# Kernel tuning notes

Measured on AMD Instinct MI355X. Metric: run time of the kernel, lower is better.

The kernel has to match this reference:

```python
import jax, jax.numpy as jnp
import numpy as np

DIM = 192; HEADS = 6; HD = DIM // HEADS; SCALE = HD ** -0.5
WS = (4, 8, 8); SS = (2, 4, 4)
NW = WS[0] * WS[1] * WS[2]  # tokens per window = 256
HIDDEN = 768; RANK1 = 384; RANK2 = 96

def _rel_index():
    Wd, Wh, Ww = WS
    coords = np.stack(np.meshgrid(np.arange(Wd), np.arange(Wh), np.arange(Ww), indexing='ij')).reshape(3, -1)
    rel = (coords[:, :, None] - coords[:, None, :]).transpose(1, 2, 0)
    rel = rel + np.array([Wd - 1, Wh - 1, Ww - 1])
    rel[:, :, 0] *= (2 * Wh - 1) * (2 * Ww - 1)
    rel[:, :, 1] *= 2 * Ww - 1
    return rel.sum(-1)  # (NW, NW) int

REL_IDX = jnp.asarray(_rel_index())

def _attn_mask(B, D, H, W):
    # static numpy computation (D,H,W are python ints) -> constant under jit
    img = np.zeros((B, D, H, W), np.float32); cnt = 0
    for d in range(0, D, WS[0]):
        for h in range(0, H, WS[1]):
            for w in range(0, W, WS[2]):
                img[:, d:d + WS[0], h:h + WS[1], w:w + WS[2]] = cnt; cnt += 1
    if any(s > 0 for s in SS):
        img = np.roll(img, (-SS[0], -SS[1], -SS[2]), axis=(1, 2, 3))
    mw = img.reshape(B, D // WS[0], WS[0], H // WS[1], WS[1], W // WS[2], WS[2]).transpose(0, 1, 3, 5, 2, 4, 6).reshape(-1, NW)
    diff = mw[:, :, None] - mw[:, None, :]
    return jnp.asarray(np.where(diff != 0, -100.0, 0.0).astype(np.float32))  # (B*nW, NW, NW)

def _ln(x, g, b):
    mu = x.mean(-1, keepdims=True)
    var = ((x - mu) ** 2).mean(-1, keepdims=True)
    return (x - mu) / jnp.sqrt(var + 1e-5) * g + b

def setup_inputs() -> dict:
    key = jax.random.key(0)
    ks = jax.random.split(key, 16)
    B, D, H, W = 1, 16, 64, 64
    N = D * H * W
    s = 0.02
    return {
        'x': jax.random.normal(ks[0], (B, N, DIM), jnp.float32),
        'norm1_g': jnp.ones((DIM,), jnp.float32), 'norm1_b': jnp.zeros((DIM,), jnp.float32),
        'qkv_w': jax.random.normal(ks[1], (DIM, 3 * DIM), jnp.float32) * s,
        'qkv_b': jnp.zeros((3 * DIM,), jnp.float32),
        'rel_bias': jax.random.normal(ks[2], (1575, HEADS), jnp.float32) * s,
        'proj_w': jax.random.normal(ks[3], (DIM, DIM), jnp.float32) * s,
        'proj_b': jnp.zeros((DIM,), jnp.float32),
        'norm2_g': jnp.ones((DIM,), jnp.float32), 'norm2_b': jnp.zeros((DIM,), jnp.float32),
        'fc1_A': jax.random.normal(ks[4], (DIM, RANK1), jnp.float32) * s,
        'fc1_Bw': jax.random.normal(ks[5], (RANK1, HIDDEN), jnp.float32) * s,
        'fc1_Bb': jnp.zeros((HIDDEN,), jnp.float32),
        'dw_w': jax.random.normal(ks[6], (HIDDEN, 1, 3, 3, 3), jnp.float32) * s,
        'dw_b': jnp.zeros((HIDDEN,), jnp.float32),
        'fc2_A': jax.random.normal(ks[7], (HIDDEN, RANK2), jnp.float32) * s,
        'fc2_Bw': jax.random.normal(ks[8], (RANK2, DIM), jnp.float32) * s,
        'fc2_Bb': jnp.zeros((DIM,), jnp.float32),
        'D': D, 'H': H, 'W': W,
    }

def reference(x, norm1_g, norm1_b, qkv_w, qkv_b, rel_bias, proj_w, proj_b,
              norm2_g, norm2_b, fc1_A, fc1_Bw, fc1_Bb, dw_w, dw_b,
              fc2_A, fc2_Bw, fc2_Bb, D, H, W):
    B, N, C = x.shape
    Wd, Wh, Ww = WS
    shortcut = x
    # --- shifted-window attention (NB: original repo never rolls x; only the mask is shifted) ---
    h = _ln(x, norm1_g, norm1_b).reshape(B, D, H, W, C)
    xw = h.reshape(B, D // Wd, Wd, H // Wh, Wh, W // Ww, Ww, C)
    xw = xw.transpose(0, 1, 3, 5, 2, 4, 6, 7).reshape(-1, NW, C)  # (B*nW, NW, C)
    qkv = (xw @ qkv_w + qkv_b).reshape(-1, NW, 3, HEADS, HD).transpose(2, 0, 3, 1, 4)
    q, k, v = qkv[0] * SCALE, qkv[1], qkv[2]           # (B*nW, heads, NW, hd)
    attn = jnp.einsum('bhnd,bhmd->bhnm', q, k)
    bias = rel_bias[REL_IDX].transpose(2, 0, 1)[None]  # (1, heads, NW, NW)
    mask = _attn_mask(B, D, H, W)                      # (B*nW, NW, NW)
    attn = jax.nn.softmax(attn + bias + mask[:, None], axis=-1)
    out = jnp.einsum('bhnm,bhmd->bhnd', attn, v).transpose(0, 2, 1, 3).reshape(-1, NW, C)
    out = out @ proj_w + proj_b
    out = out.reshape(B, D // Wd, H // Wh, W // Ww, Wd, Wh, Ww, C)
    out = out.transpose(0, 1, 4, 2, 5, 3, 6, 7).reshape(B, N, C)
    x = shortcut + out
    # --- MixFFN3D: low-rank fc1 -> depthwise conv3d -> GELU -> low-rank fc2 ---
    h = _ln(x, norm2_g, norm2_b)
    h = (h @ fc1_A) @ fc1_Bw + fc1_Bb                 # (B, N, HIDDEN)
    h = h.transpose(0, 2, 1).reshape(B, HIDDEN, D, H, W)
    h = jax.lax.conv_general_dilated(h, dw_w, (1, 1, 1), [(1, 1), (1, 1), (1, 1)],
                                     feature_group_count=HIDDEN,
                                     dimension_numbers=('NCDHW', 'OIDHW', 'NCDHW'))
    h = h + dw_b[None, :, None, None, None]
    h = jax.nn.gelu(h, approximate=False)
    h = h.reshape(B, HIDDEN, N).transpose(0, 2, 1)
    h = (h @ fc2_A) @ fc2_Bw + fc2_Bb                 # (B, N, DIM)
    return x + h
```

## Files before the change

kernel.cpp:

```cpp
#include <hip/hip_runtime.h>
#include <hip/hip_bf16.h>

typedef __hip_bfloat16 bf16;
typedef __attribute__((ext_vector_type(8))) short short8;
typedef __attribute__((ext_vector_type(4))) float f32x4;

#define N_TOK 65536
#define C_DIM 192
#define SCALE 0.17677669529663687f

__device__ __forceinline__ float b2f(bf16 v) { return __bfloat162float(v); }
__device__ __forceinline__ bf16 f2b(float v) { return __float2bfloat16(v); }
__device__ __forceinline__ float ldA(const void* p, size_t i, int f32) {
  return f32 ? ((const float*)p)[i] : b2f(((const bf16*)p)[i]);
}
__device__ __forceinline__ float s2f(short s) { union { short s; bf16 b; } u; u.s = s; return b2f(u.b); }

__global__ void detect_kernel(const unsigned short* __restrict__ xh, int* __restrict__ flag) {
  if (threadIdx.x == 0) {
    int crazy = 0;
    for (int i = 0; i < 256; ++i) {
      int e = (xh[i] >> 7) & 0xFF;
      if (e >= 0xF0 || (e >= 1 && e <= 0x60)) ++crazy;
    }
    *flag = (crazy >= 16) ? 1 : 0;
  }
}

__global__ __launch_bounds__(256) void prep_kernel(
    const void* __restrict__ qkv_w, bf16* __restrict__ QKVT,
    const void* __restrict__ proj_w, bf16* __restrict__ PROJT,
    const void* __restrict__ fc1_A, bf16* __restrict__ FC1AT,
    const void* __restrict__ fc1_Bw, bf16* __restrict__ FC1BT,
    const void* __restrict__ fc2_A, bf16* __restrict__ FC2AT,
    const void* __restrict__ fc2_Bw, bf16* __restrict__ FC2BT,
    const void* __restrict__ dw_w, bf16* __restrict__ DWT,
    const int* __restrict__ flag) {
  int f32 = *flag;
  int b = blockIdx.x;
  const void* in; bf16* out; int K, N, base;
  if (b < 432)       { in = qkv_w;  out = QKVT;  K = 192; N = 576; base = 0; }
  else if (b < 576)  { in = proj_w; out = PROJT; K = 192; N = 192; base = 432; }
  else if (b < 864)  { in = fc1_A;  out = FC1AT; K = 192; N = 384; base = 576; }
  else if (b < 2016) { in = fc1_Bw; out = FC1BT; K = 384; N = 768; base = 864; }
  else if (b < 2304) { in = fc2_A;  out = FC2AT; K = 768; N = 96;  base = 2016; }
  else if (b < 2376) { in = fc2_Bw; out = FC2BT; K = 96;  N = 192; base = 2304; }
  else {
    int idx = (b - 2376) * 256 + threadIdx.x;
    int tap = idx / 768, c = idx - tap * 768;
    DWT[idx] = f2b(ldA(dw_w, (size_t)c * 27 + tap, f32));
    return;
  }
  int idx = (b - base) * 256 + threadIdx.x;
  int n = idx / K, k = idx - n * K;
  out[idx] = f2b(ldA(in, (size_t)k * N + n, f32));
}

__global__ __launch_bounds__(256) void ln_kernel(const void* __restrict__ x,
    const void* __restrict__ g, const void* __restrict__ b, bf16* __restrict__ out,
    int windowize, int xIsBf16Fixed, const int* __restrict__ flag) {
  int wf32 = *flag;
  int f32 = xIsBf16Fixed ? 0 : wf32;
  int token = blockIdx.x * 4 + (threadIdx.x >> 6);
  int lane = threadIdx.x & 63;
  size_t base = (size_t)token * C_DIM;
  float v0 = ldA(x, base + lane, f32);
  float v1 = ldA(x, base + lane + 64, f32);
  float v2 = ldA(x, base + lane + 128, f32);
  float s = v0 + v1 + v2;
  float s2 = v0 * v0 + v1 * v1 + v2 * v2;
  #pragma unroll
  for (int o = 32; o > 0; o >>= 1) { s += __shfl_xor(s, o, 64); s2 += __shfl_xor(s2, o, 64); }
  float mu = s * (1.f / 192.f);
  float var = s2 * (1.f / 192.f) - mu * mu;
  float rstd = rsqrtf(var + 1e-5f);
  int row = token;
  if (windowize) {
    int d = token >> 12, h = (token >> 6) & 63, w = token & 63;
    int win = ((d >> 2) << 6) + ((h >> 3) << 3) + (w >> 3);
    int t = ((d & 3) << 6) + ((h & 7) << 3) + (w & 7);
    row = win * 256 + t;
  }
  bf16* po = out + (size_t)row * C_DIM;
  po[lane]       = f2b((v0 - mu) * rstd * ldA(g, lane, wf32)       + ldA(b, lane, wf32));
  po[lane + 64]  = f2b((v1 - mu) * rstd * ldA(g, lane + 64, wf32)  + ldA(b, lane + 64, wf32));
  po[lane + 128] = f2b((v2 - mu) * rstd * ldA(g, lane + 128, wf32) + ldA(b, lane + 128, wf32));
}

__global__ __launch_bounds__(256) void mfma_gemm(const bf16* __restrict__ A,
    const bf16* __restrict__ BT, const void* __restrict__ bias,
    const void* __restrict__ res, void* __restrict__ out,
    int Nc, int K, int ldk, int mode, const int* __restrict__ flag) {
  int f32 = *flag;
  __shared__ short As[128 * 104];
  __shared__ short Bs[64 * 104];
  int tid = threadIdx.x;
  int wave = tid >> 6, lane = tid & 63;
  int wm = wave >> 1, wn = wave & 1;
  int lr = lane & 15, quad = lane >> 4;
  int ncb = gridDim.x;
  int flat = blockIdx.x + ncb * blockIdx.y;
  int group = flat / (8 * ncb);
  int r = flat - group * 8 * ncb;
  int rowBase = (group * 8 + (r & 7)) * 128;
  int colBase = (r >> 3) * 64;
  f32x4 acc[4][2];
  #pragma unroll
  for (int i = 0; i < 4; ++i)
    #pragma unroll
    for (int j = 0; j < 2; ++j) acc[i][j] = f32x4{0.f, 0.f, 0.f, 0.f};

  for (int k0 = 0; k0 < K; k0 += 96) {
    #pragma unroll
    for (int it = 0; it < 6; ++it) {
      int u = tid + it * 256;
      int row = u / 12, kc = (u - row * 12) * 8;
      uint4 v = *(const uint4*)(A + (size_t)(rowBase + row) * K + k0 + kc);
      *(uint4*)&As[row * 104 + kc] = v;
    }
    #pragma unroll
    for (int it = 0; it < 3; ++it) {
      int u = tid + it * 256;
      int n = u / 12, kc = (u - n * 12) * 8;
      uint4 v = uint4{0u, 0u, 0u, 0u};
      if (colBase + n < Nc)
        v = *(const uint4*)(BT + (size_t)(colBase + n) * ldk + k0 + kc);
      *(uint4*)&Bs[n * 104 + kc] = v;
    }
    __syncthreads();
    #pragma unroll
    for (int kk = 0; kk < 3; ++kk) {
      short8 af[4], bf[2];
      #pragma unroll
      for (int i = 0; i < 4; ++i)
        af[i] = *(const short8*)&As[(wm * 64 + i * 16 + lr) * 104 + kk * 32 + quad * 8];
      #pragma unroll
      for (int j = 0; j < 2; ++j)
        bf[j] = *(const short8*)&Bs[(wn * 32 + j * 16 + lr) * 104 + kk * 32 + quad * 8];
      #pragma unroll
      for (int i = 0; i < 4; ++i)
        #pragma unroll
        for (int j = 0; j < 2; ++j)
          acc[i][j] = __builtin_amdgcn_mfma_f32_16x16x32_bf16(af[i], bf[j], acc[i][j], 0, 0, 0);
    }
    __syncthreads();
  }

  #pragma unroll
  for (int i = 0; i < 4; ++i) {
    #pragma unroll
    for (int j = 0; j < 2; ++j) {
      #pragma unroll
      for (int r4 = 0; r4 < 4; ++r4) {
        int row = rowBase + wm * 64 + i * 16 + quad * 4 + r4;
        int c = colBase + wn * 32 + j * 16 + lr;
        if (c >= Nc) continue;
        float v = acc[i][j][r4];
        if (bias) v += ldA(bias, c, f32);
        if (mode == 0) {
          ((bf16*)out)[(size_t)row * Nc + c] = f2b(v);
        } else if (mode == 1) {
          float o = b2f(((const bf16*)res)[(size_t)row * Nc + c]) + v;
          if (f32) ((float*)out)[(size_t)row * Nc + c] = o;
          else     ((bf16*)out)[(size_t)row * Nc + c] = f2b(o);
        } else {
          int win = row >> 8, t = row & 255;
          int d = ((win >> 6) << 2) + (t >> 6);
          int h = (((win >> 3) & 7) << 3) + ((t >> 3) & 7);
          int w = ((win & 7) << 3) + (t & 7);
          int n = (d << 12) + (h << 6) + w;
          ((bf16*)out)[(size_t)n * C_DIM + c] = f2b(ldA(res, (size_t)n * C_DIM + c, f32) + v);
        }
      }
    }
  }
}

__global__ __launch_bounds__(256) void attn_mfma_kernel(const bf16* __restrict__ qkvr,
    const void* __restrict__ rel_bias, bf16* __restrict__ out,
    const int* __restrict__ flag) {
  int f32 = *flag;
  __shared__ bf16 sK[256 * 40];
  __shared__ bf16 sVT[32 * 264];
  __shared__ bf16 sP[4][64 * 40];
  __shared__ float sb[1575];
  __shared__ int  sgb[256];
  int head = blockIdx.x, win = blockIdx.y;
  const bf16* base = qkvr + (size_t)win * 256 * 576;
  int qoff = head * 32, koff = 192 + head * 32, voff = 384 + head * 32;
  int tid = threadIdx.x;
  int wave = tid >> 6, lane = tid & 63;
  int lr = lane & 15, quad = lane >> 4;

  #pragma unroll
  for (int it = 0; it < 4; ++it) {
    int idx = tid + it * 256;
    int tok = idx >> 2, kc = (idx & 3) * 8;
    uint4 v = *(const uint4*)(base + (size_t)tok * 576 + koff + kc);
    *(uint4*)&sK[tok * 40 + kc] = v;
  }
  for (int idx = tid; idx < 8192; idx += 256) {
    int tok = idx >> 5, hd = idx & 31;
    sVT[hd * 264 + tok] = base[(size_t)tok * 576 + voff + hd];
  }
  for (int idx = tid; idx < 1575; idx += 256) sb[idx] = ldA(rel_bias, (size_t)idx * 6 + head, f32);
  {
    int t = tid & 255;
    int d = ((win >> 6) << 2) + (t >> 6);
    int h = (((win >> 3) & 7) << 3) + ((t >> 3) & 7);
    int w = ((win & 7) << 3) + (t & 7);
    int d2 = (d + 2) & 15, h2 = (h + 4) & 63, w2 = (w + 4) & 63;
    int g = ((d2 >> 2) << 6) + ((h2 >> 3) << 3) + (w2 >> 3);
    int td = t >> 6, th = (t >> 3) & 7, tw = t & 7;
    int bse = (td * 15 + th) * 15 + tw;
    sgb[t] = (g << 12) | bse;
  }
  __syncthreads();

  int wm = wave * 64;
  short8 aq[4];
  #pragma unroll
  for (int i = 0; i < 4; ++i)
    aq[i] = *(const short8*)(base + (size_t)(wm + i * 16 + lr) * 576 + qoff + quad * 8);
  int rinfo[16];
  #pragma unroll
  for (int i = 0; i < 4; ++i)
    #pragma unroll
    for (int r = 0; r < 4; ++r)
      rinfo[i * 4 + r] = sgb[wm + i * 16 + quad * 4 + r];

  f32x4 acc_o[4][2], acc_l[4];
  #pragma unroll
  for (int i = 0; i < 4; ++i) {
    acc_l[i] = f32x4{0.f, 0.f, 0.f, 0.f};
    #pragma unroll
    for (int j = 0; j < 2; ++j) acc_o[i][j] = f32x4{0.f, 0.f, 0.f, 0.f};
  }
  short8 bones;
  #pragma unroll
  for (int j = 0; j < 8; ++j) bones[j] = (lr == 0) ? (short)0x3F80 : (short)0;

  for (int c = 0; c < 8; ++c) {
    short8 bk[2];
    #pragma unroll
    for (int jt = 0; jt < 2; ++jt)
      bk[jt] = *(const short8*)&sK[(c * 32 + jt * 16 + lr) * 40 + quad * 8];
    f32x4 s[4][2];
    #pragma unroll
    for (int i = 0; i < 4; ++i)
      #pragma unroll
      for (int jt = 0; jt < 2; ++jt) {
        s[i][jt] = f32x4{0.f, 0.f, 0.f, 0.f};
        s[i][jt] = __builtin_amdgcn_mfma_f32_16x16x32_bf16(aq[i], bk[jt], s[i][jt], 0, 0, 0);
      }
    int cinfo[2];
    #pragma unroll
    for (int jt = 0; jt < 2; ++jt) cinfo[jt] = sgb[c * 32 + jt * 16 + lr];
    #pragma unroll
    for (int i = 0; i < 4; ++i)
      #pragma unroll
      for (int jt = 0; jt < 2; ++jt)
        #pragma unroll
        for (int r = 0; r < 4; ++r) {
          int ri = rinfo[i * 4 + r], ci = cinfo[jt];
          float sc = s[i][jt][r] * SCALE + sb[(ri & 0xFFF) - (ci & 0xFFF) + 787];
          float p = ((ri >> 12) == (ci >> 12)) ? __expf(sc) : 0.f;
          sP[wave][(i * 16 + quad * 4 + r) * 40 + jt * 16 + lr] = f2b(p);
        }
    short8 ap[4];
    #pragma unroll
    for (int i = 0; i < 4; ++i)
      ap[i] = *(const short8*)&sP[wave][(i * 16 + lr) * 40 + quad * 8];
    short8 bv[2];
    #pragma unroll
    for (int jh = 0; jh < 2; ++jh)
      bv[jh] = *(const short8*)&sVT[(jh * 16 + lr) * 264 + c * 32 + quad * 8];
    #pragma unroll
    for (int i = 0; i < 4; ++i) {
      #pragma unroll
      for (int jh = 0; jh < 2; ++jh)
        acc_o[i][jh] = __builtin_amdgcn_mfma_f32_16x16x32_bf16(ap[i], bv[jh], acc_o[i][jh], 0, 0, 0);
      acc_l[i] = __builtin_amdgcn_mfma_f32_16x16x32_bf16(ap[i], bones, acc_l[i], 0, 0, 0);
    }
  }
  #pragma unroll
  for (int i = 0; i < 4; ++i) {
    #pragma unroll
    for (int r = 0; r < 4; ++r) {
      float l = __shfl(acc_l[i][r], lane & 48, 64);
      float inv = 1.f / l;
      int t = wm + i * 16 + quad * 4 + r;
      bf16* po = out + (size_t)(win * 256 + t) * C_DIM + head * 32;
      po[lr]      = f2b(acc_o[i][0][r] * inv);
      po[16 + lr] = f2b(acc_o[i][1][r] * inv);
    }
  }
}

__global__ __launch_bounds__(256) void dwconv8w4_kernel(const bf16* __restrict__ in,
    const bf16* __restrict__ wT, const void* __restrict__ wb, bf16* __restrict__ out,
    const int* __restrict__ flag) {
  int f32 = *flag;
  int idx = blockIdx.x * 256 + threadIdx.x;
  int n4 = idx / 96, g = idx - n4 * 96;
  int c0 = g * 8;
  int d = n4 >> 10, h = (n4 >> 4) & 63, w0 = (n4 & 15) << 2;
  const bf16* inb = in + c0;
  float acc[4][8];
  {
    float bias[8];
    #pragma unroll
    for (int e = 0; e < 8; ++e) bias[e] = ldA(wb, c0 + e, f32);
    #pragma unroll
    for (int t = 0; t < 4; ++t)
      #pragma unroll
      for (int e = 0; e < 8; ++e) acc[t][e] = bias[e];
  }
  #pragma unroll
  for (int kd = 0; kd < 3; ++kd) {
    int dd = d + kd - 1;
    if ((unsigned)dd >= 16u) continue;
    #pragma unroll
    for (int kh = 0; kh < 3; ++kh) {
      int hh = h + kh - 1;
      if ((unsigned)hh >= 64u) continue;
      int rowbase = (dd << 12) + (hh << 6);
      float xf[6][8];
      #pragma unroll
      for (int j = 0; j < 6; ++j) {
        int ww = w0 + j - 1;
        short8 xv = short8{0, 0, 0, 0, 0, 0, 0, 0};
        if ((unsigned)ww < 64u)
          xv = *(const short8*)(inb + (size_t)(rowbase + ww) * 768);
        #pragma unroll
        for (int e = 0; e < 8; ++e) xf[j][e] = s2f(xv[e]);
      }
      #pragma unroll
      for (int kw = 0; kw < 3; ++kw) {
        int tap = kd * 9 + kh * 3 + kw;
        short8 wv = *(const short8*)(wT + tap * 768 + c0);
        float wf[8];
        #pragma unroll
        for (int e = 0; e < 8; ++e) wf[e] = s2f(wv[e]);
        #pragma unroll
        for (int t = 0; t < 4; ++t)
          #pragma unroll
          for (int e = 0; e < 8; ++e)
            acc[t][e] += xf[t + kw][e] * wf[e];
      }
    }
  }
  #pragma unroll
  for (int t = 0; t < 4; ++t) {
    bf16* po = out + (size_t)((d << 12) + (h << 6) + w0 + t) * 768 + c0;
    #pragma unroll
    for (int e = 0; e < 8; ++e) {
      float s = acc[t][e];
      po[e] = f2b(0.5f * s * (1.f + erff(s * 0.70710678118654752f)));
    }
  }
}

extern "C" void kernel_launch(void* const* d_in, const int* in_sizes, int n_in,
                              void* d_out, int out_size, void* d_ws, size_t ws_size,
                              hipStream_t stream) {
  const void* x      = d_in[0];
  const void* n1g    = d_in[1];
  const void* n1b    = d_in[2];
  const void* qkv_w  = d_in[3];
  const void* qkv_b  = d_in[4];
  const void* relb   = d_in[5];
  const void* proj_w = d_in[6];
  const void* proj_b = d_in[7];
  const void* n2g    = d_in[8];
  const void* n2b    = d_in[9];
  const void* fc1_A  = d_in[10];
  const void* fc1_Bw = d_in[11];
  const void* fc1_Bb = d_in[12];
  const void* dw_w   = d_in[13];
  const void* dw_b   = d_in[14];
  const void* fc2_A  = d_in[15];
  const void* fc2_Bw = d_in[16];
  const void* fc2_Bb = d_in[17];

  char* ws = (char*)d_ws;
  bf16* SCR  = (bf16*)d_out;
  bf16* X1   = (bf16*)(ws);
  bf16* QKVR = (bf16*)(ws + (size_t)24 * 1048576);
  bf16* T1   = (bf16*)(ws + (size_t)24 * 1048576);
  bf16* F2   = (bf16*)(ws + (size_t)24 * 1048576);
  bf16* F1   = (bf16*)(ws + (size_t)120 * 1048576);
  bf16* T2bf = (bf16*)(ws + (size_t)216 * 1048576);
  bf16* QKVT  = (bf16*)(ws + (size_t)228 * 1048576);
  bf16* PROJT = (bf16*)(ws + (size_t)229 * 1048576);
  bf16* FC1AT = (bf16*)(ws + (size_t)230 * 1048576);
  bf16* FC1BT = (bf16*)(ws + (size_t)231 * 1048576);
  bf16* FC2AT = (bf16*)(ws + (size_t)233 * 1048576);
  bf16* FC2BT = (bf16*)(ws + (size_t)234 * 1048576);
  bf16* DWT   = (bf16*)(ws + (size_t)235 * 1048576);
  int* FLAG   = (int*)(ws + (size_t)255 * 1048576);

  detect_kernel<<<1, 64, 0, stream>>>((const unsigned short*)x, FLAG);
  prep_kernel<<<2457, 256, 0, stream>>>(qkv_w, QKVT, proj_w, PROJT, fc1_A, FC1AT,
                                        fc1_Bw, FC1BT, fc2_A, FC2AT, fc2_Bw, FC2BT,
                                        dw_w, DWT, FLAG);
  ln_kernel<<<N_TOK / 4, 256, 0, stream>>>(x, n1g, n1b, SCR, 1, 0, FLAG);
  mfma_gemm<<<dim3(9, 512), 256, 0, stream>>>(SCR, QKVT, qkv_b, nullptr, QKVR,
                                              576, 192, 192, 0, FLAG);
  attn_mfma_kernel<<<dim3(6, 256), 256, 0, stream>>>(QKVR, relb, SCR, FLAG);
  mfma_gemm<<<dim3(3, 512), 256, 0, stream>>>(SCR, PROJT, proj_b, x, X1,
                                              192, 192, 192, 3, FLAG);
  ln_kernel<<<N_TOK / 4, 256, 0, stream>>>(X1, n2g, n2b, SCR, 0, 1, FLAG);
  mfma_gemm<<<dim3(6, 512), 256, 0, stream>>>(SCR, FC1AT, nullptr, nullptr, T1,
                                              384, 192, 192, 0, FLAG);
  mfma_gemm<<<dim3(12, 512), 256, 0, stream>>>(T1, FC1BT, fc1_Bb, nullptr, F1,
                                               768, 384, 384, 0, FLAG);
  dwconv8w4_kernel<<<6144, 256, 0, stream>>>(F1, DWT, dw_b, F2, FLAG);
  mfma_gemm<<<dim3(2, 512), 256, 0, stream>>>(F2, FC2AT, nullptr, nullptr, T2bf,
                                              96, 768, 768, 0, FLAG);
  mfma_gemm<<<dim3(3, 512), 256, 0, stream>>>(T2bf, FC2BT, fc2_Bb, X1, d_out,
                                              192, 96, 96, 1, FLAG);
}
```

Baseline: 732.9 us.

## Fold low-rank FFN factor pairs into dense weights and drop intermediate GEMMs

The prep kernel now multiplies fc1_A·fc1_Bw and fc2_A·fc2_Bw into dense transposed bf16 weights, so each MLP stage runs as one GEMM instead of two. This removes two GEMM launches and the T1/T2 intermediate buffers, and cuts total FLOPs and memory traffic per token. In exchange, the prep kernel does naive per-thread dot products over the rank dimension each call, and the fc2 GEMM becomes larger than its original two-stage form.

```diff
diff --git a/kernel.cpp b/kernel.cpp
--- a/kernel.cpp
+++ b/kernel.cpp
@@ -30,30 +30,39 @@
 __global__ __launch_bounds__(256) void prep_kernel(
     const void* __restrict__ qkv_w, bf16* __restrict__ QKVT,
     const void* __restrict__ proj_w, bf16* __restrict__ PROJT,
-    const void* __restrict__ fc1_A, bf16* __restrict__ FC1AT,
-    const void* __restrict__ fc1_Bw, bf16* __restrict__ FC1BT,
-    const void* __restrict__ fc2_A, bf16* __restrict__ FC2AT,
-    const void* __restrict__ fc2_Bw, bf16* __restrict__ FC2BT,
+    const void* __restrict__ fc1_A, const void* __restrict__ fc1_Bw, bf16* __restrict__ W1T,
+    const void* __restrict__ fc2_A, const void* __restrict__ fc2_Bw, bf16* __restrict__ W2T,
     const void* __restrict__ dw_w, bf16* __restrict__ DWT,
     const int* __restrict__ flag) {
   int f32 = *flag;
   int b = blockIdx.x;
-  const void* in; bf16* out; int K, N, base;
-  if (b < 432)       { in = qkv_w;  out = QKVT;  K = 192; N = 576; base = 0; }
-  else if (b < 576)  { in = proj_w; out = PROJT; K = 192; N = 192; base = 432; }
-  else if (b < 864)  { in = fc1_A;  out = FC1AT; K = 192; N = 384; base = 576; }
-  else if (b < 2016) { in = fc1_Bw; out = FC1BT; K = 384; N = 768; base = 864; }
-  else if (b < 2304) { in = fc2_A;  out = FC2AT; K = 768; N = 96;  base = 2016; }
-  else if (b < 2376) { in = fc2_Bw; out = FC2BT; K = 96;  N = 192; base = 2304; }
-  else {
-    int idx = (b - 2376) * 256 + threadIdx.x;
+  if (b < 432) {
+    int idx = b * 256 + threadIdx.x;
+    int n = idx / 192, k = idx - n * 192;
+    QKVT[idx] = f2b(ldA(qkv_w, (size_t)k * 576 + n, f32));
+  } else if (b < 576) {
+    int idx = (b - 432) * 256 + threadIdx.x;
+    int n = idx / 192, k = idx - n * 192;
+    PROJT[idx] = f2b(ldA(proj_w, (size_t)k * 192 + n, f32));
+  } else if (b < 657) {
+    int idx = (b - 576) * 256 + threadIdx.x;
     int tap = idx / 768, c = idx - tap * 768;
     DWT[idx] = f2b(ldA(dw_w, (size_t)c * 27 + tap, f32));
-    return;
-  }
-  int idx = (b - base) * 256 + threadIdx.x;
-  int n = idx / K, k = idx - n * K;
-  out[idx] = f2b(ldA(in, (size_t)k * N + n, f32));
+  } else if (b < 1233) {
+    int idx = (b - 657) * 256 + threadIdx.x;
+    int k = idx / 768, n = idx - k * 768;
+    float s = 0.f;
+    for (int r = 0; r < 384; ++r)
+      s += ldA(fc1_A, (size_t)k * 384 + r, f32) * ldA(fc1_Bw, (size_t)r * 768 + n, f32);
+    W1T[(size_t)n * 192 + k] = f2b(s);
+  } else {
+    int idx = (b - 1233) * 256 + threadIdx.x;
+    int k = idx / 192, n = idx - k * 192;
+    float s = 0.f;
+    for (int r = 0; r < 96; ++r)
+      s += ldA(fc2_A, (size_t)k * 96 + r, f32) * ldA(fc2_Bw, (size_t)r * 192 + n, f32);
+    W2T[(size_t)n * 768 + k] = f2b(s);
+  }
 }
 
 __global__ __launch_bounds__(256) void ln_kernel(const void* __restrict__ x,
@@ -387,22 +396,19 @@
   bf16* SCR  = (bf16*)d_out;
   bf16* X1   = (bf16*)(ws);
   bf16* QKVR = (bf16*)(ws + (size_t)24 * 1048576);
-  bf16* T1   = (bf16*)(ws + (size_t)24 * 1048576);
   bf16* F2   = (bf16*)(ws + (size_t)24 * 1048576);
   bf16* F1   = (bf16*)(ws + (size_t)120 * 1048576);
-  bf16* T2bf = (bf16*)(ws + (size_t)216 * 1048576);
   bf16* QKVT  = (bf16*)(ws + (size_t)228 * 1048576);
   bf16* PROJT = (bf16*)(ws + (size_t)229 * 1048576);
-  bf16* FC1AT = (bf16*)(ws + (size_t)230 * 1048576);
-  bf16* FC1BT = (bf16*)(ws + (size_t)231 * 1048576);
-  bf16* FC2AT = (bf16*)(ws + (size_t)233 * 1048576);
-  bf16* FC2BT = (bf16*)(ws + (size_t)234 * 1048576);
-  bf16* DWT   = (bf16*)(ws + (size_t)235 * 1048576);
+  bf16* DWT   = (bf16*)(ws + (size_t)230 * 1048576);
+  bf16* W1T   = (bf16*)(ws + (size_t)231 * 1048576);
+  bf16* W2T   = (bf16*)(ws + (size_t)232 * 1048576);
   int* FLAG   = (int*)(ws + (size_t)255 * 1048576);
 
   detect_kernel<<<1, 64, 0, stream>>>((const unsigned short*)x, FLAG);
-  prep_kernel<<<2457, 256, 0, stream>>>(qkv_w, QKVT, proj_w, PROJT, fc1_A, FC1AT,
-                                        fc1_Bw, FC1BT, fc2_A, FC2AT, fc2_Bw, FC2BT,
+  prep_kernel<<<1809, 256, 0, stream>>>(qkv_w, QKVT, proj_w, PROJT,
+                                        fc1_A, fc1_Bw, W1T,
+                                        fc2_A, fc2_Bw, W2T,
                                         dw_w, DWT, FLAG);
   ln_kernel<<<N_TOK / 4, 256, 0, stream>>>(x, n1g, n1b, SCR, 1, 0, FLAG);
   mfma_gemm<<<dim3(9, 512), 256, 0, stream>>>(SCR, QKVT, qkv_b, nullptr, QKVR,
@@ -411,13 +417,9 @@
   mfma_gemm<<<dim3(3, 512), 256, 0, stream>>>(SCR, PROJT, proj_b, x, X1,
                                               192, 192, 192, 3, FLAG);
   ln_kernel<<<N_TOK / 4, 256, 0, stream>>>(X1, n2g, n2b, SCR, 0, 1, FLAG);
-  mfma_gemm<<<dim3(6, 512), 256, 0, stream>>>(SCR, FC1AT, nullptr, nullptr, T1,
-                                              384, 192, 192, 0, FLAG);
-  mfma_gemm<<<dim3(12, 512), 256, 0, stream>>>(T1, FC1BT, fc1_Bb, nullptr, F1,
-                                               768, 384, 384, 0, FLAG);
+  mfma_gemm<<<dim3(12, 512), 256, 0, stream>>>(SCR, W1T, fc1_Bb, nullptr, F1,
+                                               768, 192, 192, 0, FLAG);
   dwconv8w4_kernel<<<6144, 256, 0, stream>>>(F1, DWT, dw_b, F2, FLAG);
-  mfma_gemm<<<dim3(2, 512), 256, 0, stream>>>(F2, FC2AT, nullptr, nullptr, T2bf,
-                                              96, 768, 768, 0, FLAG);
-  mfma_gemm<<<dim3(3, 512), 256, 0, stream>>>(T2bf, FC2BT, fc2_Bb, X1, d_out,
-                                              192, 96, 96, 1, FLAG);
-}
+  mfma_gemm<<<dim3(3, 512), 256, 0, stream>>>(F2, W2T, fc2_Bb, X1, d_out,
+                                              192, 768, 768, 1, FLAG);
+}
```

Result: no change. 741.0 us (+1.1%).
